# Kernel tuning notes

Hardware: AMD Instinct MI355X
Metric: run time of the kernel (lower is better)

## Reference

```python
import jax, jax.numpy as jnp
import numpy as np

N = 1024      # num nodes
E = 16384     # num edges
P = 8192      # num query pairs
HD1 = 64      # hidden_dim_1
HD2 = 64      # hidden_dim_2
VOCAB = 1000  # max_x + 1
EPS = 1e-5


def gcn_conv(x, W, b, src, dst, n):
    # PyG GCNConv: h = D^{-1/2} (A + I) D^{-1/2} (x @ W) + b
    h = x @ W
    loop = jnp.arange(n)
    s = jnp.concatenate([src, loop])
    d = jnp.concatenate([dst, loop])
    deg = jnp.zeros((n,), h.dtype).at[d].add(1.0)
    dis = jax.lax.rsqrt(deg)  # deg >= 1 due to self-loops
    norm = dis[s] * dis[d]
    out = jnp.zeros_like(h).at[d].add(norm[:, None] * h[s])
    return out + b


def graph_norm(x, w, b, alpha):
    # PyG GraphNorm with a single graph: stats over node dim (axis 0)
    mean = jnp.mean(x, axis=0, keepdims=True)
    sh = x - alpha * mean
    var = jnp.mean(sh * sh, axis=0, keepdims=True)
    return w * sh / jnp.sqrt(var + EPS) + b


def _forward(x_ids, ei, pos, emb, gW0, gb0, gnw0, gnb0, gna0, gW1, gb1,
             gnw1, gnb1, gna1, m1W, m1b, m2W, m2b, m3W, m3b,
             gn3w, gn3b, gn3a, ldW, ldb):
    n = x_ids.shape[0]
    src, dst = ei[0], ei[1]
    x = emb[x_ids]                                            # [n, HD1]
    # 1-WL: two GCNConv -> GraphNorm -> ReLU blocks
    x = jax.nn.relu(graph_norm(gcn_conv(x, gW0, gb0, src, dst, n), gnw0, gnb0, gna0))
    x = jax.nn.relu(graph_norm(gcn_conv(x, gW1, gb1, src, dst, n), gnw1, gnb1, gna1))
    # O(n^2) outer product: X[i,j] = x[i] * x[j]
    X = x[:, None, :] * x[None, :, :]                         # [n, n, HD1]
    eim = jnp.zeros((n, n), x.dtype).at[src, dst].set(1.0)    # adjacency indicator
    # add_chan = eye(n) @ eim = eim
    X = jnp.concatenate([X, eim[:, :, None]], axis=-1)        # [n, n, HD1+1]
    # 2-FWL refinement (layer2 = 1)
    x1 = jax.nn.relu(X @ m1W + m1b)                           # [n, n, HD2]
    x2 = jax.nn.relu(X @ m2W + m2b)                           # [n, n, HD2]
    prod = jnp.einsum('ikc,kjc->ijc', x1, x2)                 # per-channel bmm
    X = jnp.concatenate([X, prod], axis=-1)                   # [n, n, HD1+1+HD2]
    X = jax.nn.relu(graph_norm(X @ m3W + m3b, gn3w, gn3b, gn3a))
    # symmetric mul-pool then gather query pairs
    X = X * jnp.transpose(X, (1, 0, 2))                       # [n, n, HD2]
    feat = X[pos[:, 0], pos[:, 1]]                            # [P, HD2]
    return feat @ ldW + ldb                                   # [P, 1]


def setup_inputs() -> dict:
    key = jax.random.key(0)
    ks = jax.random.split(key, 12)
    sc = lambda k, s: jax.random.normal(k, s, jnp.float32) * 0.05
    d = {}
    d['x_ids'] = jax.random.randint(ks[0], (N,), 0, VOCAB)
    d['ei'] = jax.random.randint(ks[1], (2, E), 0, N)
    d['pos'] = jax.random.randint(ks[2], (P, 2), 0, N)
    d['emb'] = sc(ks[3], (VOCAB, HD1))
    d['gW0'] = sc(ks[4], (HD1, HD1)); d['gb0'] = jnp.zeros((HD1,), jnp.float32)
    d['gnw0'] = jnp.ones((HD1,), jnp.float32); d['gnb0'] = jnp.zeros((HD1,), jnp.float32); d['gna0'] = jnp.ones((HD1,), jnp.float32)
    d['gW1'] = sc(ks[5], (HD1, HD1)); d['gb1'] = jnp.zeros((HD1,), jnp.float32)
    d['gnw1'] = jnp.ones((HD1,), jnp.float32); d['gnb1'] = jnp.zeros((HD1,), jnp.float32); d['gna1'] = jnp.ones((HD1,), jnp.float32)
    d['m1W'] = sc(ks[6], (HD1 + 1, HD2)); d['m1b'] = jnp.zeros((HD2,), jnp.float32)
    d['m2W'] = sc(ks[7], (HD1 + 1, HD2)); d['m2b'] = jnp.zeros((HD2,), jnp.float32)
    d['m3W'] = sc(ks[8], (HD2 + HD1 + 1, HD2)); d['m3b'] = jnp.zeros((HD2,), jnp.float32)
    d['gn3w'] = jnp.ones((HD2,), jnp.float32); d['gn3b'] = jnp.zeros((HD2,), jnp.float32); d['gn3a'] = jnp.ones((HD2,), jnp.float32)
    d['ldW'] = sc(ks[9], (HD2, 1)); d['ldb'] = jnp.zeros((1,), jnp.float32)
    return d


def reference(x_ids, ei, pos, emb, gW0, gb0, gnw0, gnb0, gna0, gW1, gb1,
              gnw1, gnb1, gna1, m1W, m1b, m2W, m2b, m3W, m3b,
              gn3w, gn3b, gn3a, ldW, ldb):
    return _forward(x_ids, ei, pos, emb, gW0, gb0, gnw0, gnb0, gna0, gW1, gb1,
                    gnw1, gnb1, gna1, m1W, m1b, m2W, m2b, m3W, m3b,
                    gn3w, gn3b, gn3a, ldW, ldb)
```

## Files before the change

kernel.cpp:

```cpp
#include <hip/hip_runtime.h>


typedef unsigned short u16;
typedef unsigned int u32;

#define DI static __device__ __forceinline__

DI float bf2f(u16 u) { union { u32 i; float f; } v; v.i = ((u32)u) << 16; return v.f; }
DI u16 f2bf(float f) {
  union { float f; u32 i; } v; v.f = f;
  u32 u = v.i;
  return (u16)((u + 0x7fffu + ((u >> 16) & 1u)) >> 16);
}

typedef __bf16 bf16x8 __attribute__((ext_vector_type(8)));
typedef float f32x4 __attribute__((ext_vector_type(4)));

#define MFMA16(a, b, c) __builtin_amdgcn_mfma_f32_16x16x32_bf16((a), (b), (c), 0, 0, 0)

typedef const __attribute__((address_space(1))) u32* gas1;
typedef __attribute__((address_space(3))) u32* las3;


__global__ void k_setup(const int* __restrict__ xids, const float* __restrict__ emb,
                        float* __restrict__ xf, float* __restrict__ deg,
                        u32* __restrict__ eimu) {
  int g = blockIdx.x * 256 + threadIdx.x;
  if (g < 262144) eimu[g] = 0u;
  if (g < 1024) deg[g] = 1.0f;
  if (g < 65536) {
    int i = g >> 6, d = g & 63;
    xf[g] = emb[xids[i] * 64 + d];
  }
}

__global__ void k_edges(const int* __restrict__ ei, float* __restrict__ deg,
                        unsigned char* __restrict__ eim) {
  int e = blockIdx.x * 256 + threadIdx.x;
  if (e < 16384) {
    int s = ei[e], d = ei[16384 + e];
    atomicAdd(&deg[d], 1.0f);
    eim[s * 1024 + d] = 1;
  }
}

__global__ void k_gemm_node(const float* __restrict__ xf, const float* __restrict__ W,
                            const float* __restrict__ gb, const float* __restrict__ deg,
                            float* __restrict__ h, float* __restrict__ agg) {
  __shared__ float xrow[64];
  int i = blockIdx.x, c = threadIdx.x;
  xrow[c] = xf[i * 64 + c];
  __syncthreads();
  float s = 0.f;
#pragma unroll
  for (int d = 0; d < 64; ++d) s += xrow[d] * W[d * 64 + c];
  h[i * 64 + c] = s;
  agg[i * 64 + c] = s / deg[i] + gb[c];
}

__global__ void k_agg(const int* __restrict__ ei, const float* __restrict__ deg,
                      const float* __restrict__ h, float* __restrict__ agg) {
  int g = blockIdx.x * 256 + threadIdx.x;
  int e = g >> 6, c = g & 63;
  int s = ei[e], d = ei[16384 + e];
  float nrm = rsqrtf(deg[s]) * rsqrtf(deg[d]);
  atomicAdd(&agg[d * 64 + c], nrm * h[s * 64 + c]);
}

__global__ void k_gnorm(const float* __restrict__ agg, const float* __restrict__ gw,
                        const float* __restrict__ gbb, const float* __restrict__ ga,
                        float* __restrict__ xf, u16* __restrict__ xb, int last) {
  int c = blockIdx.x, t = threadIdx.x;
  float s = 0.f, ss = 0.f;
  for (int i = t; i < 1024; i += 256) {
    float v = agg[i * 64 + c];
    s += v; ss += v * v;
  }
  __shared__ float Ls[256], Lss[256];
  Ls[t] = s; Lss[t] = ss;
  __syncthreads();
  for (int off = 128; off > 0; off >>= 1) {
    if (t < off) { Ls[t] += Ls[t + off]; Lss[t] += Lss[t + off]; }
    __syncthreads();
  }
  float m = Ls[0] * (1.f / 1024.f);
  float a = ga[c];
  float var = Lss[0] * (1.f / 1024.f) - (2.f * a - a * a) * m * m;
  float sc = gw[c] * rsqrtf(fmaxf(var, 0.f) + 1e-5f);
  float bb = gbb[c];
  for (int i = t; i < 1024; i += 256) {
    float v = agg[i * 64 + c];
    float y = fmaxf(sc * (v - a * m) + bb, 0.f);
    xf[i * 64 + c] = y;
    if (last) xb[i * 64 + c] = f2bf(y);
  }
}

__global__ __launch_bounds__(256, 2) void k_build12(
    const u16* __restrict__ xbg, const unsigned char* __restrict__ eim,
    const float* __restrict__ m1W, const float* __restrict__ m1b,
    const float* __restrict__ m2W, const float* __restrict__ m2b,
    u16* __restrict__ x1tg, u16* __restrict__ x2tg, int cbase) {
  __shared__ u16 As[128 * 80];
  __shared__ u16 Bs[128 * 80];
  __shared__ u16 Cs[64 * 140];
  __shared__ unsigned char El[128 * 132];
  __shared__ float wsc[64];
  int b = blockIdx.x;
  int cg = b & 3;
  int rest = b >> 2;
  int which = rest >> 6;
  int t6 = rest & 63;
  int rbase = (t6 >> 3) * 128, sbase = (t6 & 7) * 128;
  const float* W = which ? m2W : m1W;
  const float* bias = which ? m2b : m1b;
  u16* outg = which ? x2tg : x1tg;
  int t = threadIdx.x;
  {
    int row = t >> 1, half = t & 1;
    const u32* gB = (const u32*)(xbg + (sbase + row) * 64 + half * 32);
    u32* dstB = (u32*)&Bs[row * 80 + half * 32];
#pragma unroll
    for (int k = 0; k < 16; ++k) dstB[k] = gB[k];
    int ab = which ? sbase : rbase;
    int bb = which ? rbase : sbase;
    const u32* gE = (const u32*)(eim + (size_t)(ab + row) * 1024 + bb + half * 64);
    u32* dstE = (u32*)&El[row * 132 + half * 64];
#pragma unroll
    for (int k = 0; k < 16; ++k) dstE[k] = gE[k];
  }
  int lane = t & 63, w = t >> 6;
  int q = lane >> 4, r = lane & 15;
  int wr = w >> 1, wc = w & 1;
  for (int ci = 0; ci < 4; ++ci) {
    int cl = cg * 4 + ci;
    int c = cbase + cl;
    if (t < 64) wsc[t] = W[t * 64 + c];
    __syncthreads();
    {
      int row = t >> 1, half = t & 1;
      const u32* ga = (const u32*)(xbg + (rbase + row) * 64 + half * 32);
      u32* dstA = (u32*)&As[row * 80 + half * 32];
#pragma unroll
      for (int k = 0; k < 16; ++k) {
        u32 u = ga[k];
        float f0 = bf2f((u16)(u & 0xffffu)) * wsc[half * 32 + 2 * k];
        float f1 = bf2f((u16)(u >> 16)) * wsc[half * 32 + 2 * k + 1];
        dstA[k] = (u32)f2bf(f0) | ((u32)f2bf(f1) << 16);
      }
    }
    __syncthreads();
    f32x4 z4 = {0.f, 0.f, 0.f, 0.f};
    f32x4 acc[4][4];
#pragma unroll
    for (int mi = 0; mi < 4; ++mi)
#pragma unroll
      for (int ni = 0; ni < 4; ++ni) acc[mi][ni] = z4;
#pragma unroll
    for (int ks = 0; ks < 2; ++ks) {
      bf16x8 af[4], bfr[4];
#pragma unroll
      for (int mi = 0; mi < 4; ++mi)
        af[mi] = *(const bf16x8*)&As[(wr * 64 + mi * 16 + r) * 80 + ks * 32 + q * 8];
#pragma unroll
      for (int ni = 0; ni < 4; ++ni)
        bfr[ni] = *(const bf16x8*)&Bs[(wc * 64 + ni * 16 + r) * 80 + ks * 32 + q * 8];
#pragma unroll
      for (int mi = 0; mi < 4; ++mi)
#pragma unroll
        for (int ni = 0; ni < 4; ++ni) acc[mi][ni] = MFMA16(af[mi], bfr[ni], acc[mi][ni]);
    }
    float w64 = W[64 * 64 + c];
    float bsv = bias[c];
#pragma unroll
    for (int mi = 0; mi < 4; ++mi) {
#pragma unroll
      for (int ni = 0; ni < 4; ++ni) {
        int col = wc * 64 + ni * 16 + r;
#pragma unroll
        for (int tt = 0; tt < 4; ++tt) {
          int row2 = wr * 64 + mi * 16 + q * 4 + tt;
          float e = (float)(which ? El[col * 132 + row2] : El[row2 * 132 + col]);
          acc[mi][ni][tt] = fmaxf(acc[mi][ni][tt] + e * w64 + bsv, 0.f);
        }
      }
    }
    u16* outp = outg + (size_t)cl * 1048576;
#pragma unroll
    for (int p = 0; p < 2; ++p) {
      __syncthreads();
      if (wr == p) {
#pragma unroll
        for (int mi = 0; mi < 4; ++mi)
#pragma unroll
          for (int ni = 0; ni < 4; ++ni) {
            int col = wc * 64 + ni * 16 + r;
#pragma unroll
            for (int tt = 0; tt < 4; ++tt) {
              int lrow = mi * 16 + q * 4 + tt;
              Cs[lrow * 140 + col] = f2bf(acc[mi][ni][tt]);
            }
          }
      }
      __syncthreads();
      {
        int rl = t >> 4, ch = t & 15;
#pragma unroll
        for (int it = 0; it < 4; ++it) {
          int row = it * 16 + rl;
          uint4 v = *(const uint4*)&Cs[row * 140 + ch * 8];
          *(uint4*)(outp + (size_t)(rbase + p * 64 + row) * 1024 + sbase + ch * 8) = v;
        }
      }
    }
  }
}

__global__ __launch_bounds__(256, 4) void k_prodgemm(
    const u16* __restrict__ x1tg, const u16* __restrict__ x2tg,
    u16* __restrict__ prod, int cbase) {
  __shared__ u16 pool[17408];
  int b = blockIdx.x;
  int cl = (b & 7) + ((b >> 9) << 3);
  int tile = (b >> 3) & 63;
  int i0 = (tile >> 3) * 128, j0 = (tile & 7) * 128;
  const u16* Ap = x1tg + (size_t)cl * 1048576;
  const u16* Bp = x2tg + (size_t)cl * 1048576;
  u16* Pp = prod + (size_t)(cbase + cl) * 1048576;
  int t = threadIdx.x, lane = t & 63, w = t >> 6;
  int q = lane >> 4, r = lane & 15;
  int wr = w >> 1, wc = w & 1;
  int lrow = lane >> 3, lcol = (lane & 7) * 8;
  f32x4 z4 = {0.f, 0.f, 0.f, 0.f};
  f32x4 acc[4][4];
#pragma unroll
  for (int mi = 0; mi < 4; ++mi)
#pragma unroll
    for (int ni = 0; ni < 4; ++ni) acc[mi][ni] = z4;
  for (int kk = 0; kk < 1024; kk += 64) {
    __syncthreads();
#pragma unroll
    for (int s8 = 0; s8 < 4; ++s8) {
      int rowbase = w * 32 + s8 * 8;
      int grow = rowbase + lrow;
      __builtin_amdgcn_global_load_lds(
          (gas1)(Ap + (size_t)(i0 + grow) * 1024 + kk + lcol),
          (las3)&pool[rowbase * 64], 16, 0, 0);
      __builtin_amdgcn_global_load_lds(
          (gas1)(Bp + (size_t)(j0 + grow) * 1024 + kk + lcol),
          (las3)&pool[8192 + rowbase * 64], 16, 0, 0);
    }
    __syncthreads();
#pragma unroll
    for (int ks = 0; ks < 2; ++ks) {
      bf16x8 af[4], bfr[4];
#pragma unroll
      for (int mi = 0; mi < 4; ++mi)
        af[mi] = *(const bf16x8*)&pool[(wr * 64 + mi * 16 + r) * 64 + ks * 32 + q * 8];
#pragma unroll
      for (int ni = 0; ni < 4; ++ni)
        bfr[ni] = *(const bf16x8*)&pool[8192 + (wc * 64 + ni * 16 + r) * 64 + ks * 32 + q * 8];
#pragma unroll
      for (int mi = 0; mi < 4; ++mi)
#pragma unroll
        for (int ni = 0; ni < 4; ++ni) acc[mi][ni] = MFMA16(af[mi], bfr[ni], acc[mi][ni]);
    }
  }
  __syncthreads();
#pragma unroll
  for (int mi = 0; mi < 4; ++mi)
#pragma unroll
    for (int ni = 0; ni < 4; ++ni) {
      int col = wc * 64 + ni * 16 + r;
#pragma unroll
      for (int tt = 0; tt < 4; ++tt) {
        int row2 = wr * 64 + mi * 16 + q * 4 + tt;
        pool[row2 * 136 + col] = f2bf(acc[mi][ni][tt]);
      }
    }
  __syncthreads();
  {
    int rseg = t >> 4, cseg = t & 15;
#pragma unroll
    for (int it = 0; it < 8; ++it) {
      int row = it * 16 + rseg;
      uint4 v = *(const uint4*)&pool[row * 136 + cseg * 8];
      *(uint4*)(Pp + (size_t)(i0 + row) * 1024 + j0 + cseg * 8) = v;
    }
  }
}

__global__ __launch_bounds__(256, 3) void k_buildT(
    const u16* __restrict__ xbg, const unsigned char* __restrict__ eim,
    u16* PT, const float* __restrict__ m3W, const float* __restrict__ m3b,
    float* __restrict__ S, float* __restrict__ SS) {
  __shared__ u16 A[64 * 136 + 2560];
  __shared__ u16 Wt[64 * 136];
  __shared__ unsigned char eimrow[1024];
  __shared__ float xi[64];
  int i = blockIdx.x;
  int t = threadIdx.x, lane = t & 63, w = t >> 6;
  int q = lane >> 4, r = lane & 15;
  int p4 = t >> 2, q4 = t & 3;

  uint4 pvA[2], pvB[2], xvA[2], xvB[2];
#pragma unroll
  for (int m = 0; m < 2; ++m) {
    const uint4* gp = (const uint4*)(PT + (size_t)p4 * 1048576 + (size_t)i * 1024 + m * 64 + q4 * 16);
    pvA[m] = gp[0]; pvB[m] = gp[1];
    const uint4* gx = (const uint4*)(xbg + (m * 64 + p4) * 64 + q4 * 16);
    xvA[m] = gx[0]; xvB[m] = gx[1];
  }

  {
    int zidx = i * 256 + t;
    if (zidx < 65536) { S[zidx] = 0.f; SS[zidx] = 0.f; }
  }
  if (t < 64) xi[t] = bf2f(xbg[i * 64 + t]);
  ((u32*)eimrow)[t] = ((const u32*)(eim + (size_t)i * 1024))[t];
  {
    int row = t >> 1, half = t & 1;
    int rsrc = row < 64 ? row : row + 1;
    const float4* gw = (const float4*)(m3W + rsrc * 64 + half * 32);
#pragma unroll
    for (int k = 0; k < 8; ++k) {
      float4 f = gw[k];
      Wt[(half * 32 + 4 * k + 0) * 136 + row] = f2bf(f.x);
      Wt[(half * 32 + 4 * k + 1) * 136 + row] = f2bf(f.y);
      Wt[(half * 32 + 4 * k + 2) * 136 + row] = f2bf(f.z);
      Wt[(half * 32 + 4 * k + 3) * 136 + row] = f2bf(f.w);
    }
  }
  float w64c[4], b3c[4];
#pragma unroll
  for (int ni = 0; ni < 4; ++ni) {
    int cc = ni * 16 + r;
    w64c[ni] = m3W[64 * 64 + cc];
    b3c[ni] = m3b[cc];
  }
  asm volatile("s_waitcnt lgkmcnt(0)" ::: "memory");
  __builtin_amdgcn_s_barrier();
  asm volatile("" ::: "memory");
  bf16x8 wreg[4][4];
#pragma unroll
  for (int ni = 0; ni < 4; ++ni)
#pragma unroll
    for (int ks = 0; ks < 4; ++ks)
      wreg[ni][ks] = *(const bf16x8*)&Wt[(ni * 16 + r) * 136 + ks * 32 + q * 8];
  float xiv[16];
#pragma unroll
  for (int k = 0; k < 16; ++k) xiv[k] = xi[q4 * 16 + k];

#pragma unroll 2
  for (int jc = 0; jc < 16; ++jc) {
    int s = jc & 1;
    int j0 = jc * 64;
    asm volatile("s_waitcnt lgkmcnt(0)" ::: "memory");
    __builtin_amdgcn_s_barrier();
    asm volatile("" ::: "memory");
    {
      u32 xw[8] = {xvA[s].x, xvA[s].y, xvA[s].z, xvA[s].w,
                   xvB[s].x, xvB[s].y, xvB[s].z, xvB[s].w};
      u32 ow[8];
#pragma unroll
      for (int k = 0; k < 8; ++k) {
        u32 u = xw[k];
        float f0 = bf2f((u16)(u & 0xffffu)) * xiv[2 * k];
        float f1 = bf2f((u16)(u >> 16)) * xiv[2 * k + 1];
        ow[k] = (u32)f2bf(f0) | ((u32)f2bf(f1) << 16);
      }
      uint4 lo4 = {ow[0], ow[1], ow[2], ow[3]};
      uint4 hi4 = {ow[4], ow[5], ow[6], ow[7]};
      *(uint4*)&A[p4 * 136 + q4 * 16] = lo4;
      *(uint4*)&A[p4 * 136 + q4 * 16 + 8] = hi4;
    }
    {
      u32 pw[8] = {pvA[s].x, pvA[s].y, pvA[s].z, pvA[s].w,
                   pvB[s].x, pvB[s].y, pvB[s].z, pvB[s].w};
#pragma unroll
      for (int jj = 0; jj < 16; ++jj) {
        u32 wv = pw[jj >> 1];
        u16 e = (jj & 1) ? (u16)(wv >> 16) : (u16)(wv & 0xffffu);
        A[(q4 * 16 + jj) * 136 + 64 + p4] = e;
      }
    }
    if (jc <= 13) {
      const uint4* gp = (const uint4*)(PT + (size_t)p4 * 1048576 + (size_t)i * 1024 + (j0 + 128) + q4 * 16);
      pvA[s] = gp[0]; pvB[s] = gp[1];
      const uint4* gx = (const uint4*)(xbg + (j0 + 128 + p4) * 64 + q4 * 16);
      xvA[s] = gx[0]; xvB[s] = gx[1];
    }
    asm volatile("s_waitcnt lgkmcnt(0)" ::: "memory");
    __builtin_amdgcn_s_barrier();
    asm volatile("" ::: "memory");
    f32x4 z4 = {0.f, 0.f, 0.f, 0.f};
    f32x4 acc[4];
#pragma unroll
    for (int ni = 0; ni < 4; ++ni) acc[ni] = z4;
#pragma unroll
    for (int ks = 0; ks < 4; ++ks) {
      bf16x8 af = *(const bf16x8*)&A[(w * 16 + r) * 136 + ks * 32 + q * 8];
#pragma unroll
      for (int ni = 0; ni < 4; ++ni) acc[ni] = MFMA16(af, wreg[ni][ks], acc[ni]);
    }
    u32 e4 = *(const u32*)&eimrow[j0 + w * 16 + q * 4];
#pragma unroll
    for (int ni = 0; ni < 4; ++ni) {
#pragma unroll
      for (int tt = 0; tt < 4; ++tt) {
        float ev = (float)((e4 >> (8 * tt)) & 255u);
        acc[ni][tt] = acc[ni][tt] + ev * w64c[ni] + b3c[ni];
      }
      u32 lo = (u32)f2bf(acc[ni][0]) | ((u32)f2bf(acc[ni][1]) << 16);
      u32 hi = (u32)f2bf(acc[ni][2]) | ((u32)f2bf(acc[ni][3]) << 16);
      uint2 v = {lo, hi};
      *(uint2*)(PT + (size_t)(ni * 16 + r) * 1048576 + (size_t)i * 1024 + j0 + w * 16 + q * 4) = v;
    }
  }
}

__global__ void k_stats(const u16* __restrict__ Tg, float* __restrict__ S,
                        float* __restrict__ SS) {
  int b = blockIdx.x;
  int c = b >> 3, ic = b & 7;
  int t = threadIdx.x;
  const u16* base = Tg + (size_t)c * 1048576 + (size_t)ic * 131072 + t * 4;
  float s0 = 0.f, s1 = 0.f, s2 = 0.f, s3 = 0.f;
  float q0 = 0.f, q1 = 0.f, q2 = 0.f, q3 = 0.f;
  for (int ii = 0; ii < 128; ++ii) {
    uint2 u = *(const uint2*)(base + (size_t)ii * 1024);
    float v0 = bf2f((u16)(u.x & 0xffffu)), v1 = bf2f((u16)(u.x >> 16));
    float v2 = bf2f((u16)(u.y & 0xffffu)), v3 = bf2f((u16)(u.y >> 16));
    s0 += v0; q0 += v0 * v0;
    s1 += v1; q1 += v1 * v1;
    s2 += v2; q2 += v2 * v2;
    s3 += v3; q3 += v3 * v3;
  }
  int base2 = c * 1024 + t * 4;
  atomicAdd(&S[base2 + 0], s0);
  atomicAdd(&S[base2 + 1], s1);
  atomicAdd(&S[base2 + 2], s2);
  atomicAdd(&S[base2 + 3], s3);
  atomicAdd(&SS[base2 + 0], q0);
  atomicAdd(&SS[base2 + 1], q1);
  atomicAdd(&SS[base2 + 2], q2);
  atomicAdd(&SS[base2 + 3], q3);
}

__global__ void k_statsfin(const float* __restrict__ S, const float* __restrict__ SS,
                           const float* __restrict__ gn3w, const float* __restrict__ gn3b,
                           const float* __restrict__ gn3a,
                           float* __restrict__ normA, float* __restrict__ normB) {
  int idx = blockIdx.x * 256 + threadIdx.x;
  int c = idx & 63, j = idx >> 6;
  float sum = S[c * 1024 + j];
  float ssum = SS[c * 1024 + j];
  float m = sum * (1.f / 1024.f);
  float a = gn3a[c];
  float var = ssum * (1.f / 1024.f) - (2.f * a - a * a) * m * m;
  float sc = gn3w[c] * rsqrtf(fmaxf(var, 0.f) + 1e-5f);
  normA[idx] = sc;
  normB[idx] = gn3b[c] - sc * a * m;
}

__global__ void k_final(const u16* __restrict__ Tg, const float* __restrict__ normA,
                        const float* __restrict__ normB, const int* __restrict__ pos,
                        const float* __restrict__ ldW, const float* __restrict__ ldb,
                        float* __restrict__ out) {
  int t = threadIdx.x, w = t >> 6, lane = t & 63;
  int p = blockIdx.x * 4 + w;
  int i = pos[2 * p], j = pos[2 * p + 1];
  float t1 = bf2f(Tg[(size_t)lane * 1048576 + (size_t)i * 1024 + j]);
  float y1 = fmaxf(normA[j * 64 + lane] * t1 + normB[j * 64 + lane], 0.f);
  float t2 = bf2f(Tg[(size_t)lane * 1048576 + (size_t)j * 1024 + i]);
  float y2 = fmaxf(normA[i * 64 + lane] * t2 + normB[i * 64 + lane], 0.f);
  float z = y1 * y2 * ldW[lane];
#pragma unroll
  for (int off = 32; off > 0; off >>= 1) z += __shfl_down(z, off, 64);
  if (lane == 0) out[p] = z + ldb[0];
}

extern "C" void kernel_launch(void* const* d_in, const int* in_sizes, int n_in,
                              void* d_out, int out_size, void* d_ws, size_t ws_size,
                              hipStream_t stream) {
  const int* xids   = (const int*)d_in[0];
  const int* ei     = (const int*)d_in[1];
  const int* pos    = (const int*)d_in[2];
  const float* emb  = (const float*)d_in[3];
  const float* gW0  = (const float*)d_in[4];
  const float* gb0  = (const float*)d_in[5];
  const float* gnw0 = (const float*)d_in[6];
  const float* gnb0 = (const float*)d_in[7];
  const float* gna0 = (const float*)d_in[8];
  const float* gW1  = (const float*)d_in[9];
  const float* gb1  = (const float*)d_in[10];
  const float* gnw1 = (const float*)d_in[11];
  const float* gnb1 = (const float*)d_in[12];
  const float* gna1 = (const float*)d_in[13];
  const float* m1W  = (const float*)d_in[14];
  const float* m1b  = (const float*)d_in[15];
  const float* m2W  = (const float*)d_in[16];
  const float* m2b  = (const float*)d_in[17];
  const float* m3W  = (const float*)d_in[18];
  const float* m3b  = (const float*)d_in[19];
  const float* gn3w = (const float*)d_in[20];
  const float* gn3b = (const float*)d_in[21];
  const float* gn3a = (const float*)d_in[22];
  const float* ldW  = (const float*)d_in[23];
  const float* ldb  = (const float*)d_in[24];

  char* ws = (char*)d_ws;
  float* xf   = (float*)(ws + 0);
  float* h    = (float*)(ws + 262144);
  float* agg  = (float*)(ws + 524288);
  float* deg  = (float*)(ws + 786432);
  u16*   xb   = (u16*)(ws + 790528);
  unsigned char* eim = (unsigned char*)(ws + 921600);
  float* normA = (float*)(ws + 1970176);
  float* normB = (float*)(ws + 2232320);
  u16* x1tg = (u16*)(ws + 2494464);
  u16* x2tg = (u16*)(ws + 36048896);
  u16* prod = (u16*)(ws + 69603328);
  float* Sp  = (float*)x1tg;
  float* SSp = Sp + 65536;
  float* out = (float*)d_out;

  k_setup<<<1024, 256, 0, stream>>>(xids, emb, xf, deg, (u32*)eim);
  k_edges<<<64, 256, 0, stream>>>(ei, deg, eim);
  k_gemm_node<<<1024, 64, 0, stream>>>(xf, gW0, gb0, deg, h, agg);
  k_agg<<<4096, 256, 0, stream>>>(ei, deg, h, agg);
  k_gnorm<<<64, 256, 0, stream>>>(agg, gnw0, gnb0, gna0, xf, xb, 0);
  k_gemm_node<<<1024, 64, 0, stream>>>(xf, gW1, gb1, deg, h, agg);
  k_agg<<<4096, 256, 0, stream>>>(ei, deg, h, agg);
  k_gnorm<<<64, 256, 0, stream>>>(agg, gnw1, gnb1, gna1, xf, xb, 1);
  for (int g = 0; g < 4; ++g) {
    k_build12<<<512, 256, 0, stream>>>(xb, eim, m1W, m1b, m2W, m2b, x1tg, x2tg, g * 16);
    k_prodgemm<<<1024, 256, 0, stream>>>(x1tg, x2tg, prod, g * 16);
  }
  k_buildT<<<1024, 256, 0, stream>>>(xb, eim, prod, m3W, m3b, Sp, SSp);
  k_stats<<<512, 256, 0, stream>>>(prod, Sp, SSp);
  k_statsfin<<<256, 256, 0, stream>>>(Sp, SSp, gn3w, gn3b, gn3a, normA, normB);
  k_final<<<2048, 256, 0, stream>>>(prod, normA, normB, pos, ldW, ldb, out);
}
```

Before: 517.3 us.

## Restructure buildT: fold xi into weights, async LDS x loads, staged stores

The k_buildT kernel is reorganized. The per-row x_i scaling is folded into the m3W weight tile, so the per-chunk elementwise multiply on x_j goes away. The x_j tiles are now fetched with global_load_lds into double-buffered, XOR-swizzled shared memory. The edge-indicator and bias terms are computed as an extra MFMA instead of scalar FMAs, and outputs are staged in LDS so they can be written back as coalesced 16-byte stores one chunk later. The intent is to cut VALU work, bank conflicts and uncoalesced global writes, at the cost of tighter manual vmcnt scheduling and one extra MFMA per tile.

```diff
diff --git a/kernel.cpp b/kernel.cpp
--- a/kernel.cpp
+++ b/kernel.cpp
@@ -294,127 +294,188 @@
     const u16* __restrict__ xbg, const unsigned char* __restrict__ eim,
     u16* PT, const float* __restrict__ m3W, const float* __restrict__ m3b,
     float* __restrict__ S, float* __restrict__ SS) {
-  __shared__ u16 A[64 * 136 + 2560];
-  __shared__ u16 Wt[64 * 136];
-  __shared__ unsigned char eimrow[1024];
-  __shared__ float xi[64];
+  __shared__ u16 pool[20736];
+  u16* XL0 = pool;
+  u16* XL1 = pool + 4096;
+  u16* XRb = pool + 8192;
+  u16* Wt  = pool;
+  u16* stg = pool + 12288;
+  unsigned char* eimrow = (unsigned char*)(pool + 16896);
+
   int i = blockIdx.x;
   int t = threadIdx.x, lane = t & 63, w = t >> 6;
   int q = lane >> 4, r = lane & 15;
-  int p4 = t >> 2, q4 = t & 3;
-
-  uint4 pvA[2], pvB[2], xvA[2], xvB[2];
-#pragma unroll
-  for (int m = 0; m < 2; ++m) {
-    const uint4* gp = (const uint4*)(PT + (size_t)p4 * 1048576 + (size_t)i * 1024 + m * 64 + q4 * 16);
-    pvA[m] = gp[0]; pvB[m] = gp[1];
-    const uint4* gx = (const uint4*)(xbg + (m * 64 + p4) * 64 + q4 * 16);
-    xvA[m] = gx[0]; xvB[m] = gx[1];
-  }
-
+  int rx = r & 7;
+
+  uint4 pvA0, pvB0, pvA1, pvB1;
+  {
+    const uint4* gp = (const uint4*)(PT + (size_t)lane * 1048576 + (size_t)i * 1024 + 0 + w * 16);
+    pvA0 = gp[0]; pvB0 = gp[1];
+  }
+  {
+    const uint4* gp = (const uint4*)(PT + (size_t)lane * 1048576 + (size_t)i * 1024 + 64 + w * 16);
+    pvA1 = gp[0]; pvB1 = gp[1];
+  }
   {
     int zidx = i * 256 + t;
     if (zidx < 65536) { S[zidx] = 0.f; SS[zidx] = 0.f; }
   }
-  if (t < 64) xi[t] = bf2f(xbg[i * 64 + t]);
   ((u32*)eimrow)[t] = ((const u32*)(eim + (size_t)i * 1024))[t];
   {
     int row = t >> 1, half = t & 1;
     int rsrc = row < 64 ? row : row + 1;
+    float xsc = (row < 64) ? bf2f(xbg[i * 64 + row]) : 1.f;
     const float4* gw = (const float4*)(m3W + rsrc * 64 + half * 32);
 #pragma unroll
     for (int k = 0; k < 8; ++k) {
       float4 f = gw[k];
-      Wt[(half * 32 + 4 * k + 0) * 136 + row] = f2bf(f.x);
-      Wt[(half * 32 + 4 * k + 1) * 136 + row] = f2bf(f.y);
-      Wt[(half * 32 + 4 * k + 2) * 136 + row] = f2bf(f.z);
-      Wt[(half * 32 + 4 * k + 3) * 136 + row] = f2bf(f.w);
-    }
-  }
-  float w64c[4], b3c[4];
+      Wt[(half * 32 + 4 * k + 0) * 136 + row] = f2bf(f.x * xsc);
+      Wt[(half * 32 + 4 * k + 1) * 136 + row] = f2bf(f.y * xsc);
+      Wt[(half * 32 + 4 * k + 2) * 136 + row] = f2bf(f.z * xsc);
+      Wt[(half * 32 + 4 * k + 3) * 136 + row] = f2bf(f.w * xsc);
+    }
+  }
+  bf16x8 wregE[4];
 #pragma unroll
   for (int ni = 0; ni < 4; ++ni) {
     int cc = ni * 16 + r;
-    w64c[ni] = m3W[64 * 64 + cc];
-    b3c[ni] = m3b[cc];
+    u16 wb = f2bf(m3W[64 * 64 + cc]);
+    u16 bb = f2bf(m3b[cc]);
+    union { u16 a[8]; bf16x8 v; } u;
+#pragma unroll
+    for (int z = 0; z < 8; ++z) u.a[z] = 0;
+    if (q == 0) { u.a[0] = wb; u.a[1] = bb; }
+    wregE[ni] = u.v;
   }
   asm volatile("s_waitcnt lgkmcnt(0)" ::: "memory");
   __builtin_amdgcn_s_barrier();
   asm volatile("" ::: "memory");
-  bf16x8 wreg[4][4];
+  bf16x8 wregL[4][2], wregR[4][2];
 #pragma unroll
   for (int ni = 0; ni < 4; ++ni)
 #pragma unroll
-    for (int ks = 0; ks < 4; ++ks)
-      wreg[ni][ks] = *(const bf16x8*)&Wt[(ni * 16 + r) * 136 + ks * 32 + q * 8];
-  float xiv[16];
-#pragma unroll
-  for (int k = 0; k < 16; ++k) xiv[k] = xi[q4 * 16 + k];
-
-#pragma unroll 2
-  for (int jc = 0; jc < 16; ++jc) {
-    int s = jc & 1;
-    int j0 = jc * 64;
-    asm volatile("s_waitcnt lgkmcnt(0)" ::: "memory");
-    __builtin_amdgcn_s_barrier();
-    asm volatile("" ::: "memory");
-    {
-      u32 xw[8] = {xvA[s].x, xvA[s].y, xvA[s].z, xvA[s].w,
-                   xvB[s].x, xvB[s].y, xvB[s].z, xvB[s].w};
-      u32 ow[8];
-#pragma unroll
-      for (int k = 0; k < 8; ++k) {
-        u32 u = xw[k];
-        float f0 = bf2f((u16)(u & 0xffffu)) * xiv[2 * k];
-        float f1 = bf2f((u16)(u >> 16)) * xiv[2 * k + 1];
-        ow[k] = (u32)f2bf(f0) | ((u32)f2bf(f1) << 16);
-      }
-      uint4 lo4 = {ow[0], ow[1], ow[2], ow[3]};
-      uint4 hi4 = {ow[4], ow[5], ow[6], ow[7]};
-      *(uint4*)&A[p4 * 136 + q4 * 16] = lo4;
-      *(uint4*)&A[p4 * 136 + q4 * 16 + 8] = hi4;
-    }
-    {
-      u32 pw[8] = {pvA[s].x, pvA[s].y, pvA[s].z, pvA[s].w,
-                   pvB[s].x, pvB[s].y, pvB[s].z, pvB[s].w};
-#pragma unroll
-      for (int jj = 0; jj < 16; ++jj) {
-        u32 wv = pw[jj >> 1];
-        u16 e = (jj & 1) ? (u16)(wv >> 16) : (u16)(wv & 0xffffu);
-        A[(q4 * 16 + jj) * 136 + 64 + p4] = e;
-      }
-    }
-    if (jc <= 13) {
-      const uint4* gp = (const uint4*)(PT + (size_t)p4 * 1048576 + (size_t)i * 1024 + (j0 + 128) + q4 * 16);
-      pvA[s] = gp[0]; pvB[s] = gp[1];
-      const uint4* gx = (const uint4*)(xbg + (j0 + 128 + p4) * 64 + q4 * 16);
-      xvA[s] = gx[0]; xvB[s] = gx[1];
-    }
-    asm volatile("s_waitcnt lgkmcnt(0)" ::: "memory");
-    __builtin_amdgcn_s_barrier();
-    asm volatile("" ::: "memory");
-    f32x4 z4 = {0.f, 0.f, 0.f, 0.f};
-    f32x4 acc[4];
-#pragma unroll
-    for (int ni = 0; ni < 4; ++ni) acc[ni] = z4;
-#pragma unroll
-    for (int ks = 0; ks < 4; ++ks) {
-      bf16x8 af = *(const bf16x8*)&A[(w * 16 + r) * 136 + ks * 32 + q * 8];
-#pragma unroll
-      for (int ni = 0; ni < 4; ++ni) acc[ni] = MFMA16(af, wreg[ni][ks], acc[ni]);
-    }
-    u32 e4 = *(const u32*)&eimrow[j0 + w * 16 + q * 4];
-#pragma unroll
-    for (int ni = 0; ni < 4; ++ni) {
-#pragma unroll
-      for (int tt = 0; tt < 4; ++tt) {
-        float ev = (float)((e4 >> (8 * tt)) & 255u);
-        acc[ni][tt] = acc[ni][tt] + ev * w64c[ni] + b3c[ni];
-      }
-      u32 lo = (u32)f2bf(acc[ni][0]) | ((u32)f2bf(acc[ni][1]) << 16);
-      u32 hi = (u32)f2bf(acc[ni][2]) | ((u32)f2bf(acc[ni][3]) << 16);
-      uint2 v = {lo, hi};
-      *(uint2*)(PT + (size_t)(ni * 16 + r) * 1048576 + (size_t)i * 1024 + j0 + w * 16 + q * 4) = v;
+    for (int ks = 0; ks < 2; ++ks) {
+      wregL[ni][ks] = *(const bf16x8*)&Wt[(ni * 16 + r) * 136 + ks * 32 + q * 8];
+      wregR[ni][ks] = *(const bf16x8*)&Wt[(ni * 16 + r) * 136 + (ks + 2) * 32 + q * 8];
+    }
+  asm volatile("s_waitcnt lgkmcnt(0)" ::: "memory");
+  __builtin_amdgcn_sched_barrier(0);
+  __builtin_amdgcn_s_barrier();
+  asm volatile("" ::: "memory");
+  {
+#pragma unroll
+    for (int bb = 0; bb < 2; ++bb) {
+      int b = w * 2 + bb;
+      int srow = b * 8 + (lane >> 3);
+      int skb = (lane & 7) ^ ((lane >> 3) & 7);
+      __builtin_amdgcn_global_load_lds((gas1)(xbg + srow * 64 + skb * 8),
+                                       (las3)(XL0 + b * 512), 16, 0, 0);
+    }
+  }
+
+#define BT_BODY(JC, SS_, VMC, DUMP)                                           \
+  {                                                                           \
+    const int jc = (JC);                                                      \
+    const int j0 = jc * 64;                                                   \
+    asm volatile("s_waitcnt lgkmcnt(0)" ::: "memory");                        \
+    __builtin_amdgcn_s_barrier();                                             \
+    asm volatile("" ::: "memory");                                            \
+    if (DUMP) {      \
+      int pl = t >> 3, off = (t & 7) * 8;                                     \
+      _Pragma("unroll")                                                       \
+      for (int kk = 0; kk < 2; ++kk) {                                        \
+        int plane = kk * 32 + pl;                                             \
+        uint4 v = *(const uint4*)&stg[plane * 72 + off];                      \
+        *(uint4*)(PT + (size_t)plane * 1048576 + (size_t)i * 1024 +           \
+                  (j0 - 64) + off) = v;                                       \
+      }                                                                       \
+    }                                                                         \
+    {         \
+      u32 pw[8] = {pvA##SS_.x, pvA##SS_.y, pvA##SS_.z, pvA##SS_.w,            \
+                   pvB##SS_.x, pvB##SS_.y, pvB##SS_.z, pvB##SS_.w};           \
+      _Pragma("unroll")                                                       \
+      for (int jj = 0; jj < 16; ++jj) {                                       \
+        u32 wv = pw[jj >> 1];                                                 \
+        u16 e = (jj & 1) ? (u16)(wv >> 16) : (u16)wv;                         \
+        XRb[(w * 16 + jj) * 64 + (((lane >> 3) ^ (jj & 7)) << 3) +            \
+            (lane & 7)] = e;                                                  \
+      }                                                                       \
+    }                                                                         \
+    {              \
+      int jn = ((jc + 2) & 15) * 64;                                          \
+      const uint4* gp = (const uint4*)(PT + (size_t)lane * 1048576 +          \
+                                       (size_t)i * 1024 + jn + w * 16);       \
+      pvA##SS_ = gp[0]; pvB##SS_ = gp[1];                                     \
+    }                                                                         \
+    {                        \
+      int jn = ((jc + 1) & 15) * 64;                                          \
+      u16* xld = (SS_) ? XL0 : XL1;                                           \
+      _Pragma("unroll")                                                       \
+      for (int bb = 0; bb < 2; ++bb) {                                        \
+        int b = w * 2 + bb;                                                   \
+        int srow = jn + b * 8 + (lane >> 3);                                  \
+        int skb = (lane & 7) ^ ((lane >> 3) & 7);                             \
+        __builtin_amdgcn_global_load_lds((gas1)(xbg + srow * 64 + skb * 8),   \
+                                         (las3)(xld + b * 512), 16, 0, 0);    \
+      }                                                                       \
+    }                                                                         \
+    asm volatile("s_waitcnt vmcnt(" #VMC ") lgkmcnt(0)" ::: "memory");        \
+    __builtin_amdgcn_s_barrier();                                             \
+    asm volatile("" ::: "memory");                                            \
+    {                                \
+      const u16* XLc = (SS_) ? XL1 : XL0;                                     \
+      int rbase = (w * 16 + r) * 64;                                          \
+      bf16x8 xlf[2], xrf[2];                                                  \
+      _Pragma("unroll")                                                       \
+      for (int ks = 0; ks < 2; ++ks) {                                        \
+        xlf[ks] = *(const bf16x8*)&XLc[rbase + (((ks * 4 + q) ^ rx) << 3)];   \
+        xrf[ks] = *(const bf16x8*)&XRb[rbase + (((ks * 4 + q) ^ rx) << 3)];   \
+      }                                                                       \
+      unsigned char ev = eimrow[j0 + w * 16 + r];                             \
+      union { u16 a[8]; bf16x8 v; } ue;                                       \
+      _Pragma("unroll")                                                       \
+      for (int z = 0; z < 8; ++z) ue.a[z] = 0;                                \
+      if (q == 0) {                                                           \
+        ue.a[0] = ev ? (u16)0x3F80 : (u16)0;                                  \
+        ue.a[1] = (u16)0x3F80;                                                \
+      }                                                                       \
+      bf16x8 de = ue.v;                                                       \
+      f32x4 z4 = {0.f, 0.f, 0.f, 0.f};                                        \
+      _Pragma("unroll")                                                       \
+      for (int ni = 0; ni < 4; ++ni) {                                        \
+        f32x4 acc = z4;                                                       \
+        acc = MFMA16(xlf[0], wregL[ni][0], acc);                              \
+        acc = MFMA16(xlf[1], wregL[ni][1], acc);                              \
+        acc = MFMA16(xrf[0], wregR[ni][0], acc);                              \
+        acc = MFMA16(xrf[1], wregR[ni][1], acc);                              \
+        acc = MFMA16(de, wregE[ni], acc);                                     \
+        u32 lo = (u32)f2bf(acc[0]) | ((u32)f2bf(acc[1]) << 16);               \
+        u32 hi = (u32)f2bf(acc[2]) | ((u32)f2bf(acc[3]) << 16);               \
+        uint2 vv; vv.x = lo; vv.y = hi;                                       \
+        *(uint2*)&stg[(ni * 16 + r) * 72 + w * 16 + q * 4] = vv;              \
+      }                                                                       \
+    }                                                                         \
+  }
+
+  BT_BODY(0, 0, 4, 0);
+#pragma unroll 1
+  for (int jp = 0; jp < 7; ++jp) {
+    BT_BODY(2 * jp + 1, 1, 6, 1);
+    BT_BODY(2 * jp + 2, 0, 6, 1);
+  }
+  BT_BODY(15, 1, 6, 1);
+#undef BT_BODY
+
+  asm volatile("s_waitcnt lgkmcnt(0)" ::: "memory");
+  __builtin_amdgcn_s_barrier();
+  asm volatile("" ::: "memory");
+  {
+    int pl = t >> 3, off = (t & 7) * 8;
+#pragma unroll
+    for (int kk = 0; kk < 2; ++kk) {
+      int plane = kk * 32 + pl;
+      uint4 v = *(const uint4*)&stg[plane * 72 + off];
+      *(uint4*)(PT + (size_t)plane * 1048576 + (size_t)i * 1024 + 960 + off) = v;
     }
   }
 }
```

Result: no change. 524.5 us (+1.4%).
